# Performance work log

Hardware: AMD Instinct MI355X
Metric: run time of the kernel (lower is better)

## Reference

```python
import jax, jax.numpy as jnp
import numpy as np

# LIFRefracParameters defaults (norse)
TAU_SYN_INV = 200.0   # 1/5e-3
TAU_MEM_INV = 100.0   # 1/1e-2
V_LEAK = 0.0
V_TH = 1.0
V_RESET = 0.0
ALPHA = 100.0
RHO_RESET = 5.0
DT = 0.001


@jax.custom_vjp
def heaviside(x):
    # forward: hard threshold; backward: super-spike surrogate
    return (x > 0).astype(x.dtype)

def _heaviside_fwd(x):
    return heaviside(x), x

def _heaviside_bwd(x, g):
    return (g / (ALPHA * jnp.abs(x) + 1.0) ** 2,)

heaviside.defvjp(_heaviside_fwd, _heaviside_bwd)


def setup_inputs() -> dict:
    key = jax.random.key(0)
    ks = jax.random.split(key, 8)
    B, H, I = 32768, 256, 128
    return {
        "input_tensor": jax.random.normal(ks[0], (B, I), dtype=jnp.float32),
        "z": jax.random.uniform(ks[1], (B, H), dtype=jnp.float32),
        "v": jax.random.normal(ks[2], (B, H), dtype=jnp.float32),
        "i": jax.random.normal(ks[3], (B, H), dtype=jnp.float32),
        "rho": jnp.zeros((B, H), dtype=jnp.float32),
        "input_weights": jax.random.normal(ks[4], (H, I), dtype=jnp.float32) / np.sqrt(I),
        "recurrent_weights": jax.random.normal(ks[5], (H, H), dtype=jnp.float32) / np.sqrt(H),
        "g_coupling": jax.random.normal(ks[6], (H, H), dtype=jnp.float32) / np.sqrt(H),
    }


def reference(input_tensor, z, v, i, rho, input_weights, recurrent_weights, g_coupling):
    # --- lif_mc_step ---
    # membrane decay + multi-compartment coupling
    dv = DT * TAU_MEM_INV * ((V_LEAK - v) + i) + v @ g_coupling.T
    v_decayed = v + dv
    # synaptic current decay
    i_decayed = i + (-DT * TAU_SYN_INV) * i
    # spike
    z_new = heaviside(v_decayed - V_TH)
    v_new = (1.0 - z_new) * v_decayed + z_new * V_RESET
    i_new = i_decayed + input_tensor @ input_weights.T + z @ recurrent_weights.T
    # --- refractory update ---
    refrac_mask = heaviside(rho)
    v_new = (1.0 - refrac_mask) * v_new + refrac_mask * v
    z_new = (1.0 - refrac_mask) * z_new
    rho_new = (1.0 - z_new) * jax.nn.relu(rho - refrac_mask) + z_new * RHO_RESET
    return z_new, v_new, i_new, rho_new
```

## Files before the change

### kernel.cpp

```cpp
#include <hip/hip_runtime.h>

typedef __attribute__((ext_vector_type(8))) _Float16 f16x8;
typedef __attribute__((ext_vector_type(4))) _Float16 f16x4;
typedef __attribute__((ext_vector_type(4))) float    f32x4;

constexpr int Bsz = 32768;
constexpr int Hn  = 256;
constexpr int In  = 128;
constexpr long long BH = (long long)Bsz * Hn;

__global__ __launch_bounds__(256) void k_prep(
    const float* __restrict__ Wi, const float* __restrict__ Wr,
    const float* __restrict__ Gc, _Float16* __restrict__ ws)
{
    const int idx = blockIdx.x * 256 + threadIdx.x;
    {
        const int cg = idx >> 12, rem = idx & 4095;
        const int t = rem >> 9, l = (rem >> 3) & 63, j = idx & 7;
        const int col = cg * 16 + (l & 15);
        const int k   = t * 32 + (l >> 4) * 8 + j;
        float g = Gc[col * Hn + k];
        _Float16 gh = (_Float16)g;
        ws[idx]         = gh;
        ws[65536 + idx] = (_Float16)((g - (float)gh) * 4096.0f);
        ws[131072 + idx] = (_Float16)Wr[col * Hn + k];
    }
    if (idx < 32768) {
        const int cg = idx >> 11, rem = idx & 2047;
        const int t = rem >> 9, l = (rem >> 3) & 63, j = idx & 7;
        const int col = cg * 16 + (l & 15);
        const int k   = t * 32 + (l >> 4) * 8 + j;
        ws[196608 + idx] = (_Float16)Wi[col * In + k];
    }
}

__device__ __forceinline__ int swzV(int row, int col4) {
    return (row * 1024 + col4 * 4) ^ ((row & 7) << 4);
}
__device__ __forceinline__ int swzZ(int row, int colh) {
    return (row * 512 + colh * 2) ^ ((row & 7) << 4);
}
__device__ __forceinline__ int swzX(int row, int colh) {
    return (row * 256 + colh * 2) ^ ((row & 7) << 4);
}

__device__ __forceinline__ f16x8 cvt_hi2(float4 a, float4 b) {
    float f[8] = {a.x, a.y, a.z, a.w, b.x, b.y, b.z, b.w};
    f16x8 r;
    #pragma unroll
    for (int k = 0; k < 8; ++k) r[k] = (_Float16)f[k];
    return r;
}
__device__ __forceinline__ f16x8 cvt_mid2(float4 a, float4 b) {
    float f[8] = {a.x, a.y, a.z, a.w, b.x, b.y, b.z, b.w};
    f16x8 r;
    #pragma unroll
    for (int k = 0; k < 8; ++k) {
        _Float16 h = (_Float16)f[k];
        r[k] = (_Float16)((f[k] - (float)h) * 4096.0f);
    }
    return r;
}
__device__ __forceinline__ f16x4 cvt4h(float4 a) {
    f16x4 r;
    r[0] = (_Float16)a.x; r[1] = (_Float16)a.y;
    r[2] = (_Float16)a.z; r[3] = (_Float16)a.w;
    return r;
}

#define MFMA16(A, B, C) __builtin_amdgcn_mfma_f32_16x16x32_f16(A, B, C, 0, 0, 0)

__global__ __launch_bounds__(256, 4) void k_main(
    const float* __restrict__ x, const float* __restrict__ z,
    const float* __restrict__ v, const float* __restrict__ cur,
    const float* __restrict__ rho, const _Float16* __restrict__ ws,
    float* __restrict__ out)
{
    __shared__ char smem[32768];
    char* V  = smem;
    char* Z  = smem + 16384;
    char* X  = smem + 24576;
    char* Oc = smem;
    char* Oi = smem + 16384;

    const int tid  = threadIdx.x;
    const int lane = tid & 63;
    const int ln = lane & 15, lg = lane >> 4;
    const int wv = tid >> 6;
    const int wc = wv * 64;
    const int rowBase = blockIdx.x * 16;

    {
        const float4* vsrc = (const float4*)(v + (size_t)rowBase * Hn);
        const float4* zsrc = (const float4*)(z + (size_t)rowBase * Hn);
        const float4* xsrc = (const float4*)(x + (size_t)rowBase * In);
        #pragma unroll
        for (int k = 0; k < 4; ++k) {
            const int f = k * 256 + tid;
            const int row = f >> 6, c4 = (f & 63) * 4;
            *(float4*)(V + swzV(row, c4)) = vsrc[f];
        }
        #pragma unroll
        for (int k = 0; k < 4; ++k) {
            const int f = k * 256 + tid;
            const int row = f >> 6, c4 = (f & 63) * 4;
            *(f16x4*)(Z + swzZ(row, c4)) = cvt4h(zsrc[f]);
        }
        #pragma unroll
        for (int k = 0; k < 2; ++k) {
            const int f = k * 256 + tid;
            const int row = f >> 5, c4 = (f & 31) * 4;
            *(f16x4*)(X + swzX(row, c4)) = cvt4h(xsrc[f]);
        }
    }
    __syncthreads();

    f32x4 acc_c[4], acc_cm[4], acc_i[4];
    #pragma unroll
    for (int c = 0; c < 4; ++c) {
        acc_c[c]  = (f32x4){0.f, 0.f, 0.f, 0.f};
        acc_cm[c] = (f32x4){0.f, 0.f, 0.f, 0.f};
        acc_i[c]  = (f32x4){0.f, 0.f, 0.f, 0.f};
    }

    const _Float16* Gh  = ws;
    const _Float16* Gm  = ws + 65536;
    const _Float16* Wr  = ws + 131072;
    const _Float16* Wi  = ws + 196608;

    #pragma unroll 2
    for (int t = 0; t < 8; ++t) {
        const int kf = t * 32 + lg * 8;
        float4 va0 = *(const float4*)(V + swzV(ln, kf));
        float4 va1 = *(const float4*)(V + swzV(ln, kf + 4));
        f16x8 vh = cvt_hi2(va0, va1);
        f16x8 vm = cvt_mid2(va0, va1);
        f16x8 zh = *(const f16x8*)(Z + swzZ(ln, kf));
        f16x8 xh;
        if (t < 4) xh = *(const f16x8*)(X + swzX(ln, kf));
        #pragma unroll
        for (int c = 0; c < 4; ++c) {
            const int cg = wv * 4 + c;
            f16x8 bgh = *(const f16x8*)(Gh + ((size_t)(cg * 8 + t) * 64 + lane) * 8);
            f16x8 bgm = *(const f16x8*)(Gm + ((size_t)(cg * 8 + t) * 64 + lane) * 8);
            f16x8 bwr = *(const f16x8*)(Wr + ((size_t)(cg * 8 + t) * 64 + lane) * 8);
            acc_c[c]  = MFMA16(vh, bgh, acc_c[c]);
            acc_cm[c] = MFMA16(vh, bgm, acc_cm[c]);
            acc_cm[c] = MFMA16(vm, bgh, acc_cm[c]);
            acc_i[c]  = MFMA16(zh, bwr, acc_i[c]);
            if (t < 4) {
                f16x8 bwi = *(const f16x8*)(Wi + ((size_t)(cg * 4 + t) * 64 + lane) * 8);
                acc_i[c] = MFMA16(xh, bwi, acc_i[c]);
            }
        }
    }

    #pragma unroll
    for (int c = 0; c < 4; ++c)
        acc_c[c] = acc_c[c] + acc_cm[c] * 2.44140625e-4f;

    __syncthreads();
    #pragma unroll
    for (int c = 0; c < 4; ++c) {
        const int col = wc + c * 16 + ln;
        #pragma unroll
        for (int r = 0; r < 4; ++r) {
            *(float*)(Oc + swzV(lg * 4 + r, col)) = acc_c[c][r];
            *(float*)(Oi + swzV(lg * 4 + r, col)) = acc_i[c][r];
        }
    }

    float4 vv4[4], ii4[4], rh4[4];
    #pragma unroll
    for (int j = 0; j < 4; ++j) {
        const int f = j * 256 + tid;
        const int row = f >> 6, c4 = (f & 63) * 4;
        const size_t gidx = (size_t)(rowBase + row) * Hn + c4;
        vv4[j] = *(const float4*)(v + gidx);
        ii4[j] = *(const float4*)(cur + gidx);
        rh4[j] = *(const float4*)(rho + gidx);
    }
    __syncthreads();

    float* out_z   = out;
    float* out_v   = out + BH;
    float* out_i   = out + 2 * BH;
    float* out_rho = out + 3 * BH;

    #pragma unroll
    for (int j = 0; j < 4; ++j) {
        const int f = j * 256 + tid;
        const int row = f >> 6, c4 = (f & 63) * 4;
        const size_t gidx = (size_t)(rowBase + row) * Hn + c4;
        float4 coup = *(const float4*)(Oc + swzV(row, c4));
        float4 ai   = *(const float4*)(Oi + swzV(row, c4));
        float zn[4], vn[4], rn[4];
        float vvv[4] = {vv4[j].x, vv4[j].y, vv4[j].z, vv4[j].w};
        float iii[4] = {ii4[j].x, ii4[j].y, ii4[j].z, ii4[j].w};
        float rrr[4] = {rh4[j].x, rh4[j].y, rh4[j].z, rh4[j].w};
        float cpp[4] = {coup.x, coup.y, coup.z, coup.w};
        #pragma unroll
        for (int q = 0; q < 4; ++q) {
            float dv   = 0.1f * ((0.0f - vvv[q]) + iii[q]) + cpp[q];
            float vdec = vvv[q] + dv;
            float zf   = (vdec - 1.0f) > 0.0f ? 1.0f : 0.0f;
            float vnew = (1.0f - zf) * vdec;
            float mask = rrr[q] > 0.0f ? 1.0f : 0.0f;
            vnew = (1.0f - mask) * vnew + mask * vvv[q];
            zf   = (1.0f - mask) * zf;
            float rhon = (1.0f - zf) * fmaxf(rrr[q] - mask, 0.0f) + zf * 5.0f;
            zn[q] = zf; vn[q] = vnew; rn[q] = rhon;
        }
        *(float4*)(out_z + gidx)   = make_float4(zn[0], zn[1], zn[2], zn[3]);
        *(float4*)(out_v + gidx)   = make_float4(vn[0], vn[1], vn[2], vn[3]);
        *(float4*)(out_rho + gidx) = make_float4(rn[0], rn[1], rn[2], rn[3]);
        *(float4*)(out_i + gidx)   = make_float4(
            0.8f * iii[0] + ai.x, 0.8f * iii[1] + ai.y,
            0.8f * iii[2] + ai.z, 0.8f * iii[3] + ai.w);
    }
}

extern "C" void kernel_launch(void* const* d_in, const int* in_sizes, int n_in,
                              void* d_out, int out_size, void* d_ws, size_t ws_size,
                              hipStream_t stream) {
    const float* x   = (const float*)d_in[0];
    const float* z   = (const float*)d_in[1];
    const float* v   = (const float*)d_in[2];
    const float* cur = (const float*)d_in[3];
    const float* rho = (const float*)d_in[4];
    const float* Wi  = (const float*)d_in[5];
    const float* Wr  = (const float*)d_in[6];
    const float* Gc  = (const float*)d_in[7];
    float* out = (float*)d_out;
    _Float16* ws = (_Float16*)d_ws;

    hipLaunchKernelGGL(k_prep, dim3(256), dim3(256), 0, stream, Wi, Wr, Gc, ws);
    hipLaunchKernelGGL(k_main, dim3(Bsz / 16), dim3(256), 0, stream,
                       x, z, v, cur, rho, ws, out);
}
```

Before: 100.8 us.

## Use 32-row tiles with 8 waves and pre-split V hi/mid halves in LDS

Each block now handles 32 batch rows with 512 threads. Each wave computes two 16-row M tiles over two column groups, so every B-fragment loaded from global memory feeds two MFMAs instead of one. The fp16 hi/mid split of V is now done once during the LDS fill rather than inside the K loop by every wave. This roughly halves the weight traffic per output row, at the cost of 64KB of LDS per block and lower block-level occupancy.

```diff
diff --git a/kernel.cpp b/kernel.cpp
--- a/kernel.cpp
+++ b/kernel.cpp
@@ -34,61 +34,54 @@
     }
 }
 
-__device__ __forceinline__ int swzV(int row, int col4) {
-    return (row * 1024 + col4 * 4) ^ ((row & 7) << 4);
-}
-__device__ __forceinline__ int swzZ(int row, int colh) {
+__device__ __forceinline__ int swzH(int row, int colh) {
     return (row * 512 + colh * 2) ^ ((row & 7) << 4);
 }
 __device__ __forceinline__ int swzX(int row, int colh) {
     return (row * 256 + colh * 2) ^ ((row & 7) << 4);
 }
-
-__device__ __forceinline__ f16x8 cvt_hi2(float4 a, float4 b) {
-    float f[8] = {a.x, a.y, a.z, a.w, b.x, b.y, b.z, b.w};
-    f16x8 r;
-    #pragma unroll
-    for (int k = 0; k < 8; ++k) r[k] = (_Float16)f[k];
-    return r;
-}
-__device__ __forceinline__ f16x8 cvt_mid2(float4 a, float4 b) {
-    float f[8] = {a.x, a.y, a.z, a.w, b.x, b.y, b.z, b.w};
-    f16x8 r;
-    #pragma unroll
-    for (int k = 0; k < 8; ++k) {
-        _Float16 h = (_Float16)f[k];
-        r[k] = (_Float16)((f[k] - (float)h) * 4096.0f);
-    }
-    return r;
-}
+__device__ __forceinline__ int swzO(int row, int col4) {
+    return (row * 1024 + col4 * 4) ^ ((row & 7) << 4);
+}
+
 __device__ __forceinline__ f16x4 cvt4h(float4 a) {
     f16x4 r;
     r[0] = (_Float16)a.x; r[1] = (_Float16)a.y;
     r[2] = (_Float16)a.z; r[3] = (_Float16)a.w;
     return r;
 }
+__device__ __forceinline__ f16x4 cvt4m(float4 a) {
+    float f[4] = {a.x, a.y, a.z, a.w};
+    f16x4 r;
+    #pragma unroll
+    for (int k = 0; k < 4; ++k) {
+        _Float16 h = (_Float16)f[k];
+        r[k] = (_Float16)((f[k] - (float)h) * 4096.0f);
+    }
+    return r;
+}
 
 #define MFMA16(A, B, C) __builtin_amdgcn_mfma_f32_16x16x32_f16(A, B, C, 0, 0, 0)
 
-__global__ __launch_bounds__(256, 4) void k_main(
+__global__ __launch_bounds__(512, 4) void k_main(
     const float* __restrict__ x, const float* __restrict__ z,
     const float* __restrict__ v, const float* __restrict__ cur,
     const float* __restrict__ rho, const _Float16* __restrict__ ws,
     float* __restrict__ out)
 {
-    __shared__ char smem[32768];
-    char* V  = smem;
-    char* Z  = smem + 16384;
-    char* X  = smem + 24576;
+    __shared__ char smem[65536];
+    char* VH = smem;
+    char* VM = smem + 16384;
+    char* ZH = smem + 32768;
+    char* XH = smem + 49152;
     char* Oc = smem;
-    char* Oi = smem + 16384;
+    char* Oi = smem + 32768;
 
     const int tid  = threadIdx.x;
     const int lane = tid & 63;
     const int ln = lane & 15, lg = lane >> 4;
-    const int wv = tid >> 6;
-    const int wc = wv * 64;
-    const int rowBase = blockIdx.x * 16;
+    const int w  = tid >> 6;
+    const int rowBase = blockIdx.x * 32;
 
     {
         const float4* vsrc = (const float4*)(v + (size_t)rowBase * Hn);
@@ -96,32 +89,36 @@
         const float4* xsrc = (const float4*)(x + (size_t)rowBase * In);
         #pragma unroll
         for (int k = 0; k < 4; ++k) {
-            const int f = k * 256 + tid;
+            const int f = k * 512 + tid;
             const int row = f >> 6, c4 = (f & 63) * 4;
-            *(float4*)(V + swzV(row, c4)) = vsrc[f];
+            float4 a = vsrc[f];
+            *(f16x4*)(VH + swzH(row, c4)) = cvt4h(a);
+            *(f16x4*)(VM + swzH(row, c4)) = cvt4m(a);
         }
         #pragma unroll
         for (int k = 0; k < 4; ++k) {
-            const int f = k * 256 + tid;
+            const int f = k * 512 + tid;
             const int row = f >> 6, c4 = (f & 63) * 4;
-            *(f16x4*)(Z + swzZ(row, c4)) = cvt4h(zsrc[f]);
+            *(f16x4*)(ZH + swzH(row, c4)) = cvt4h(zsrc[f]);
         }
         #pragma unroll
         for (int k = 0; k < 2; ++k) {
-            const int f = k * 256 + tid;
+            const int f = k * 512 + tid;
             const int row = f >> 5, c4 = (f & 31) * 4;
-            *(f16x4*)(X + swzX(row, c4)) = cvt4h(xsrc[f]);
+            *(f16x4*)(XH + swzX(row, c4)) = cvt4h(xsrc[f]);
         }
     }
     __syncthreads();
 
-    f32x4 acc_c[4], acc_cm[4], acc_i[4];
-    #pragma unroll
-    for (int c = 0; c < 4; ++c) {
-        acc_c[c]  = (f32x4){0.f, 0.f, 0.f, 0.f};
-        acc_cm[c] = (f32x4){0.f, 0.f, 0.f, 0.f};
-        acc_i[c]  = (f32x4){0.f, 0.f, 0.f, 0.f};
-    }
+    f32x4 acc_c[2][2], acc_cm[2][2], acc_i[2][2];
+    #pragma unroll
+    for (int m = 0; m < 2; ++m)
+        #pragma unroll
+        for (int c = 0; c < 2; ++c) {
+            acc_c[m][c]  = (f32x4){0.f, 0.f, 0.f, 0.f};
+            acc_cm[m][c] = (f32x4){0.f, 0.f, 0.f, 0.f};
+            acc_i[m][c]  = (f32x4){0.f, 0.f, 0.f, 0.f};
+        }
 
     const _Float16* Gh  = ws;
     const _Float16* Gm  = ws + 65536;
@@ -131,49 +128,63 @@
     #pragma unroll 2
     for (int t = 0; t < 8; ++t) {
         const int kf = t * 32 + lg * 8;
-        float4 va0 = *(const float4*)(V + swzV(ln, kf));
-        float4 va1 = *(const float4*)(V + swzV(ln, kf + 4));
-        f16x8 vh = cvt_hi2(va0, va1);
-        f16x8 vm = cvt_mid2(va0, va1);
-        f16x8 zh = *(const f16x8*)(Z + swzZ(ln, kf));
-        f16x8 xh;
-        if (t < 4) xh = *(const f16x8*)(X + swzX(ln, kf));
-        #pragma unroll
-        for (int c = 0; c < 4; ++c) {
-            const int cg = wv * 4 + c;
+        f16x8 vh0 = *(const f16x8*)(VH + swzH(ln,      kf));
+        f16x8 vh1 = *(const f16x8*)(VH + swzH(ln + 16, kf));
+        f16x8 vm0 = *(const f16x8*)(VM + swzH(ln,      kf));
+        f16x8 vm1 = *(const f16x8*)(VM + swzH(ln + 16, kf));
+        f16x8 zh0 = *(const f16x8*)(ZH + swzH(ln,      kf));
+        f16x8 zh1 = *(const f16x8*)(ZH + swzH(ln + 16, kf));
+        f16x8 xh0, xh1;
+        if (t < 4) {
+            xh0 = *(const f16x8*)(XH + swzX(ln,      kf));
+            xh1 = *(const f16x8*)(XH + swzX(ln + 16, kf));
+        }
+        #pragma unroll
+        for (int c = 0; c < 2; ++c) {
+            const int cg = w * 2 + c;
             f16x8 bgh = *(const f16x8*)(Gh + ((size_t)(cg * 8 + t) * 64 + lane) * 8);
             f16x8 bgm = *(const f16x8*)(Gm + ((size_t)(cg * 8 + t) * 64 + lane) * 8);
             f16x8 bwr = *(const f16x8*)(Wr + ((size_t)(cg * 8 + t) * 64 + lane) * 8);
-            acc_c[c]  = MFMA16(vh, bgh, acc_c[c]);
-            acc_cm[c] = MFMA16(vh, bgm, acc_cm[c]);
-            acc_cm[c] = MFMA16(vm, bgh, acc_cm[c]);
-            acc_i[c]  = MFMA16(zh, bwr, acc_i[c]);
+            acc_c[0][c]  = MFMA16(vh0, bgh, acc_c[0][c]);
+            acc_c[1][c]  = MFMA16(vh1, bgh, acc_c[1][c]);
+            acc_cm[0][c] = MFMA16(vh0, bgm, acc_cm[0][c]);
+            acc_cm[1][c] = MFMA16(vh1, bgm, acc_cm[1][c]);
+            acc_cm[0][c] = MFMA16(vm0, bgh, acc_cm[0][c]);
+            acc_cm[1][c] = MFMA16(vm1, bgh, acc_cm[1][c]);
+            acc_i[0][c]  = MFMA16(zh0, bwr, acc_i[0][c]);
+            acc_i[1][c]  = MFMA16(zh1, bwr, acc_i[1][c]);
             if (t < 4) {
                 f16x8 bwi = *(const f16x8*)(Wi + ((size_t)(cg * 4 + t) * 64 + lane) * 8);
-                acc_i[c] = MFMA16(xh, bwi, acc_i[c]);
+                acc_i[0][c] = MFMA16(xh0, bwi, acc_i[0][c]);
+                acc_i[1][c] = MFMA16(xh1, bwi, acc_i[1][c]);
             }
         }
     }
 
     #pragma unroll
-    for (int c = 0; c < 4; ++c)
-        acc_c[c] = acc_c[c] + acc_cm[c] * 2.44140625e-4f;
+    for (int m = 0; m < 2; ++m)
+        #pragma unroll
+        for (int c = 0; c < 2; ++c)
+            acc_c[m][c] = acc_c[m][c] + acc_cm[m][c] * 2.44140625e-4f;
 
     __syncthreads();
     #pragma unroll
-    for (int c = 0; c < 4; ++c) {
-        const int col = wc + c * 16 + ln;
-        #pragma unroll
-        for (int r = 0; r < 4; ++r) {
-            *(float*)(Oc + swzV(lg * 4 + r, col)) = acc_c[c][r];
-            *(float*)(Oi + swzV(lg * 4 + r, col)) = acc_i[c][r];
-        }
-    }
+    for (int m = 0; m < 2; ++m)
+        #pragma unroll
+        for (int c = 0; c < 2; ++c) {
+            const int col = (w * 2 + c) * 16 + ln;
+            #pragma unroll
+            for (int r = 0; r < 4; ++r) {
+                const int row = m * 16 + lg * 4 + r;
+                *(float*)(Oc + swzO(row, col)) = acc_c[m][c][r];
+                *(float*)(Oi + swzO(row, col)) = acc_i[m][c][r];
+            }
+        }
 
     float4 vv4[4], ii4[4], rh4[4];
     #pragma unroll
     for (int j = 0; j < 4; ++j) {
-        const int f = j * 256 + tid;
+        const int f = j * 512 + tid;
         const int row = f >> 6, c4 = (f & 63) * 4;
         const size_t gidx = (size_t)(rowBase + row) * Hn + c4;
         vv4[j] = *(const float4*)(v + gidx);
@@ -189,11 +200,11 @@
 
     #pragma unroll
     for (int j = 0; j < 4; ++j) {
-        const int f = j * 256 + tid;
+        const int f = j * 512 + tid;
         const int row = f >> 6, c4 = (f & 63) * 4;
         const size_t gidx = (size_t)(rowBase + row) * Hn + c4;
-        float4 coup = *(const float4*)(Oc + swzV(row, c4));
-        float4 ai   = *(const float4*)(Oi + swzV(row, c4));
+        float4 coup = *(const float4*)(Oc + swzO(row, c4));
+        float4 ai   = *(const float4*)(Oi + swzO(row, c4));
         float zn[4], vn[4], rn[4];
         float vvv[4] = {vv4[j].x, vv4[j].y, vv4[j].z, vv4[j].w};
         float iii[4] = {ii4[j].x, ii4[j].y, ii4[j].z, ii4[j].w};
@@ -235,6 +246,6 @@
     _Float16* ws = (_Float16*)d_ws;
 
     hipLaunchKernelGGL(k_prep, dim3(256), dim3(256), 0, stream, Wi, Wr, Gc, ws);
-    hipLaunchKernelGGL(k_main, dim3(Bsz / 16), dim3(256), 0, stream,
+    hipLaunchKernelGGL(k_main, dim3(Bsz / 32), dim3(512), 0, stream,
                        x, z, v, cur, rho, ws, out);
 }
```

Result: faster. 80.78 us (-19.9%).
